# Performance work log

Measured on AMD Instinct MI355X. Metric: run time of the kernel, lower is better.

Reference implementation:

```python
import jax, jax.numpy as jnp
import numpy as np

B, S, E = 2, 2048, 2048
H, KV, D = 16, 4, 128
G = H // KV  # query heads per kv head
THETA = 10000.0


def setup_inputs() -> dict:
    key = jax.random.key(0)
    ks = jax.random.split(key, 5)
    scale = 0.02
    return {
        "x": jax.random.normal(ks[0], (B, S, E), dtype=jnp.float32),
        "Wq": jax.random.normal(ks[1], (E, H * D), dtype=jnp.float32) * scale,
        "Wk": jax.random.normal(ks[2], (E, KV * D), dtype=jnp.float32) * scale,
        "Wv": jax.random.normal(ks[3], (E, KV * D), dtype=jnp.float32) * scale,
        "Wo": jax.random.normal(ks[4], (E, E), dtype=jnp.float32) * scale,
    }


def _rope_tables(seq_len, head_dim, theta):
    inv_freq = 1.0 / theta ** (jnp.arange(0, head_dim, 2, dtype=jnp.float32) / head_dim)
    t = jnp.arange(seq_len, dtype=jnp.float32)
    freqs = jnp.outer(t, inv_freq)  # [S, D/2]
    cos = jnp.concatenate([jnp.cos(freqs), jnp.cos(freqs)], axis=-1)  # [S, D]
    sin = jnp.concatenate([jnp.sin(freqs), jnp.sin(freqs)], axis=-1)
    return cos, sin


def _apply_rope(x, cos, sin):
    # x: [B, h, S, D]; cos/sin: [S, D] broadcast over batch/heads
    d2 = x.shape[-1] // 2
    x1, x2 = x[..., :d2], x[..., d2:]
    rotated = jnp.concatenate([-x2, x1], axis=-1)
    return x * cos + rotated * sin


def reference(x, Wq, Wk, Wv, Wo):
    b, s, _ = x.shape
    q = (x @ Wq).reshape(b, s, H, D).transpose(0, 2, 1, 3)   # [B,H,S,D]
    k = (x @ Wk).reshape(b, s, KV, D).transpose(0, 2, 1, 3)  # [B,KV,S,D]
    v = (x @ Wv).reshape(b, s, KV, D).transpose(0, 2, 1, 3)

    cos, sin = _rope_tables(s, D, THETA)
    q = _apply_rope(q, cos, sin)
    k = _apply_rope(k, cos, sin)

    # GQA: q head h attends to kv head h // G (repeat_interleave order)
    qg = q.reshape(b, KV, G, s, D)
    scores = jnp.einsum("bkgsd,bktd->bkgst", qg, k) / jnp.sqrt(jnp.asarray(D, x.dtype))
    causal = jnp.tril(jnp.ones((s, s), dtype=bool))
    scores = jnp.where(causal, scores, jnp.asarray(-jnp.inf, scores.dtype))
    attn = jax.nn.softmax(scores, axis=-1)
    out = jnp.einsum("bkgst,bktd->bkgsd", attn, v)  # [B,KV,G,S,D]
    out = out.reshape(b, H, s, D).transpose(0, 2, 1, 3).reshape(b, s, H * D)
    return out @ Wo
```

## Files before the change

### kernel.cpp

```cpp
#include <hip/hip_runtime.h>
#include <stdint.h>

#define B_ 2
#define S_ 2048
#define E_ 2048
#define H_ 16
#define KV_ 4
#define D_ 128
#define G_ (H_ / KV_)
#define M_ (B_ * S_)

typedef unsigned short u16;
typedef unsigned int u32;
typedef __bf16 bf16x8 __attribute__((ext_vector_type(8)));
typedef float f32x4 __attribute__((ext_vector_type(4)));

__device__ __forceinline__ u16 f2bf(float f) {
  __bf16 h = (__bf16)f;
  return *(u16*)&h;
}
__device__ __forceinline__ float bf2f(u16 x) {
  return __uint_as_float(((u32)x) << 16);
}
__device__ __forceinline__ void store_c(u16* p, float v) { *p = f2bf(v); }
__device__ __forceinline__ void store_c(float* p, float v) { *p = v; }

__device__ __forceinline__ void gload_lds16(const u16* g, u16* lds) {
  __builtin_amdgcn_global_load_lds((const __attribute__((address_space(1))) u32*)g,
                                   (__attribute__((address_space(3))) u32*)lds,
                                   16, 0, 0);
}

__global__ __launch_bounds__(256) void convert_fp32_bf16(const float4* __restrict__ x,
                                                         uint2* __restrict__ o, int n4) {
  int i = blockIdx.x * 256 + threadIdx.x;
  if (i >= n4) return;
  float4 v = x[i];
  uint2 r;
  r.x = (u32)f2bf(v.x) | ((u32)f2bf(v.y) << 16);
  r.y = (u32)f2bf(v.z) | ((u32)f2bf(v.w) << 16);
  o[i] = r;
}

__global__ __launch_bounds__(256) void transpose_conv_w(const float* __restrict__ W,
                                                        u16* __restrict__ Wt,
                                                        int Kdim, int Ndim) {
  __shared__ float tile[32][33];
  int n0 = blockIdx.x * 32, k0 = blockIdx.y * 32;
  int tx = threadIdx.x, ty = threadIdx.y;
#pragma unroll
  for (int i = 0; i < 4; i++) {
    int r = ty + i * 8;
    tile[r][tx] = W[(size_t)(k0 + r) * Ndim + n0 + tx];
  }
  __syncthreads();
#pragma unroll
  for (int i = 0; i < 4; i++) {
    int r = ty + i * 8;
    Wt[(size_t)(n0 + r) * Kdim + k0 + tx] = f2bf(tile[tx][r]);
  }
}

__global__ __launch_bounds__(256) void transpose_v(const u16* __restrict__ V,
                                                   u16* __restrict__ Vt) {
  __shared__ u16 tile[32][33];
  int bkv = blockIdx.z;
  int b = bkv / KV_, kv = bkv % KV_;
  int s0 = blockIdx.x * 32, d0 = blockIdx.y * 32;
  int tx = threadIdx.x, ty = threadIdx.y;
#pragma unroll
  for (int i = 0; i < 4; i++) {
    int r = ty + i * 8;
    tile[r][tx] = V[((size_t)((b * S_ + s0 + r) * KV_ + kv)) * D_ + d0 + tx];
  }
  __syncthreads();
#pragma unroll
  for (int i = 0; i < 4; i++) {
    int r = ty + i * 8;
    Vt[((size_t)(b * KV_ + kv) * D_ + d0 + r) * S_ + s0 + tx] = tile[tx][r];
  }
}

__global__ __launch_bounds__(256) void rope_k_repack(const u16* __restrict__ Kin,
                                                     u16* __restrict__ Kp, int total) {
  int idx = blockIdx.x * 256 + threadIdx.x;
  if (idx >= total) return;
  int d = idx & 63;
  int rem = idx >> 6;
  int kv = rem % KV_;
  int row = rem / KV_;
  int b = row >> 11;
  int spos = row & (S_ - 1);
  size_t src = ((size_t)row * KV_ + kv) * D_ + d;
  float x0 = bf2f(Kin[src]);
  float x1 = bf2f(Kin[src + 64]);
  float ang = (float)spos * expf(-0.14391156831212787f * (float)d);
  float sn, cs;
  sincosf(ang, &sn, &cs);
  size_t dst = ((size_t)((b * KV_ + kv) * S_ + spos)) * D_ + d;
  Kp[dst]      = f2bf(x0 * cs - x1 * sn);
  Kp[dst + 64] = f2bf(x1 * cs + x0 * sn);
}

template <typename CT>
__device__ __forceinline__ void gemm_body(const u16* __restrict__ A, const u16* __restrict__ Bt,
                                          CT* __restrict__ C, int Kdim, int Ndim,
                                          int m0, int n0) {
  __shared__ __align__(16) u16 As[128 * 32];
  __shared__ __align__(16) u16 Bs[128 * 32];
  const int tid = threadIdx.x;
  const int lane = tid & 63;
  const int wave = tid >> 6;
  const int wm = wave >> 1, wn = wave & 1;
  const int quad = lane >> 4, lm = lane & 15;
  const int srow = tid >> 2;
  const int scol = (tid & 3) * 8;

  f32x4 zero = {0.f, 0.f, 0.f, 0.f};
  f32x4 acc[4][4];
#pragma unroll
  for (int i = 0; i < 4; i++)
#pragma unroll
    for (int j = 0; j < 4; j++) acc[i][j] = zero;

  const u16* gA = A + (size_t)(m0 + srow) * Kdim + scol;
  const u16* gB = Bt + (size_t)(n0 + srow) * Kdim + scol;
  const size_t rstep = (size_t)64 * Kdim;
  u16* ldsA0 = As + wave * 512;
  u16* ldsA1 = As + 2048 + wave * 512;
  u16* ldsB0 = Bs + wave * 512;
  u16* ldsB1 = Bs + 2048 + wave * 512;

  for (int k0 = 0; k0 < Kdim; k0 += 32) {
    gload_lds16(gA + k0, ldsA0);
    gload_lds16(gA + k0 + rstep, ldsA1);
    gload_lds16(gB + k0, ldsB0);
    gload_lds16(gB + k0 + rstep, ldsB1);
    __syncthreads();
    bf16x8 af[4], bfr[4];
#pragma unroll
    for (int mt = 0; mt < 4; mt++)
      af[mt] = *(const bf16x8*)(As + (wm * 64 + mt * 16 + lm) * 32 + quad * 8);
#pragma unroll
    for (int nt = 0; nt < 4; nt++)
      bfr[nt] = *(const bf16x8*)(Bs + (wn * 64 + nt * 16 + lm) * 32 + quad * 8);
#pragma unroll
    for (int mt = 0; mt < 4; mt++)
#pragma unroll
      for (int nt = 0; nt < 4; nt++)
        acc[mt][nt] = __builtin_amdgcn_mfma_f32_16x16x32_bf16(af[mt], bfr[nt], acc[mt][nt], 0, 0, 0);
    __syncthreads();
  }

#pragma unroll
  for (int mt = 0; mt < 4; mt++) {
    const int row = m0 + wm * 64 + mt * 16 + quad * 4;
#pragma unroll
    for (int nt = 0; nt < 4; nt++) {
      const int col = n0 + wn * 64 + nt * 16 + lm;
#pragma unroll
      for (int r = 0; r < 4; r++)
        store_c(C + (size_t)(row + r) * Ndim + col, acc[mt][nt][r]);
    }
  }
}

template <typename CT>
__global__ __launch_bounds__(256) void gemm_bt_kernel(const u16* __restrict__ A,
                                                      const u16* __restrict__ Bt,
                                                      CT* __restrict__ C, int Ndim, int Kdim) {
  gemm_body<CT>(A, Bt, C, Kdim, Ndim, blockIdx.y * 128, blockIdx.x * 128);
}

__global__ __launch_bounds__(256) void gemm_qkv_kernel(const u16* __restrict__ A,
                                                       const u16* __restrict__ WqT,
                                                       const u16* __restrict__ WkT,
                                                       const u16* __restrict__ WvT,
                                                       u16* __restrict__ Qb,
                                                       u16* __restrict__ Kb,
                                                       u16* __restrict__ Vb) {
  int bx = blockIdx.x;
  const u16* Bt;
  u16* C;
  int n0, Ndim;
  if (bx < 16)      { Bt = WqT; C = Qb; n0 = bx * 128;        Ndim = 2048; }
  else if (bx < 20) { Bt = WkT; C = Kb; n0 = (bx - 16) * 128; Ndim = 512; }
  else              { Bt = WvT; C = Vb; n0 = (bx - 20) * 128; Ndim = 512; }
  gemm_body<u16>(A, Bt, C, 2048, Ndim, blockIdx.y * 128, n0);
}

__global__ __launch_bounds__(256, 2) void attn_kernel(const u16* __restrict__ Q,
                                                      const u16* __restrict__ Kp,
                                                      const u16* __restrict__ Vt,
                                                      u16* __restrict__ O) {
  __shared__ __align__(16) u16 Ksh[2][64 * 128];
  __shared__ __align__(16) u16 Vsh[128 * 64];
  __shared__ __align__(16) u16 Psh[4][16 * 64];

  const int tid = threadIdx.x;
  const int lane = tid & 63;
  const int wave = tid >> 6;
  const int quad = lane >> 4, lm = lane & 15;
  const int b = blockIdx.z, h = blockIdx.y;
  const int kh = h / G_;

  const u16* Kbase = Kp + (size_t)(b * KV_ + kh) * S_ * D_;
  const u16* Vbase = Vt + (size_t)(b * KV_ + kh) * D_ * S_;
  u16* pw = &Psh[wave][0];

  int offK[4], offV[4], ldsOff[4];
#pragma unroll
  for (int i = 0; i < 4; i++) {
    int idx = (wave * 4 + i) * 64 + lane;
    int rK = idx >> 4;
    int cK = (idx & 15) ^ (rK & 7);
    offK[i] = rK * 128 + cK * 8;
    int rV = idx >> 3;
    int cV = (idx & 7) ^ (rV & 7);
    offV[i] = rV * S_ + cV * 8;
    ldsOff[i] = (wave * 4 + i) * 512;
  }

  bf16x8 onesb;
#pragma unroll
  for (int j = 0; j < 8; j++) onesb[j] = (__bf16)1.0f;

#pragma unroll
  for (int half = 0; half < 2; half++) {
    const int qi = half ? blockIdx.x : (31 - blockIdx.x);
    const int sq0 = qi * 64;
    const int nT = qi + 1;
    const int wrow = sq0 + wave * 16;

    const int spos = wrow + lm;
    const u16* qptr = Q + ((size_t)(b * S_ + wrow + lm) * H_ + h) * D_;
    bf16x8 qf[4];
#pragma unroll
    for (int ks = 0; ks < 2; ks++) {
      bf16x8 a = *(const bf16x8*)(qptr + ks * 32 + quad * 8);
      bf16x8 c = *(const bf16x8*)(qptr + (ks + 2) * 32 + quad * 8);
#pragma unroll
      for (int j = 0; j < 8; j++) {
        int d = ks * 32 + quad * 8 + j;
        float ang = (float)spos * __expf(-0.14391156831212787f * (float)d);
        float sn, cs;
        sincosf(ang, &sn, &cs);
        float x0 = (float)a[j], x1 = (float)c[j];
        const float scale = 0.08838834764831845f;
        qf[ks][j]     = (__bf16)((x0 * cs - x1 * sn) * scale);
        qf[ks + 2][j] = (__bf16)((x1 * cs + x0 * sn) * scale);
      }
    }

    f32x4 o[8];
    f32x4 lacc = {0.f, 0.f, 0.f, 0.f};
#pragma unroll
    for (int i = 0; i < 8; i++) o[i] = f32x4{0.f, 0.f, 0.f, 0.f};

    __syncthreads();
#pragma unroll
    for (int i = 0; i < 4; i++)
      gload_lds16(Kbase + offK[i], &Ksh[0][ldsOff[i]]);

    for (int t = 0; t < nT; t++) {
      const int sk0 = t << 6;
      const bool act = (sk0 <= wrow + 15);
      __syncthreads();

      if (t + 1 < nT) {
        const u16* kg = Kbase + (size_t)(t + 1) * 64 * 128;
        u16* kb_next = &Ksh[(t + 1) & 1][0];
#pragma unroll
        for (int i = 0; i < 4; i++)
          gload_lds16(kg + offK[i], kb_next + ldsOff[i]);
      }
#pragma unroll
      for (int i = 0; i < 4; i++)
        gload_lds16(Vbase + sk0 + offV[i], &Vsh[ldsOff[i]]);

      f32x4 sc[4];
      if (act) {
        const u16* kbuf = &Ksh[t & 1][0];
#pragma unroll
        for (int nt = 0; nt < 4; nt++) sc[nt] = f32x4{0.f, 0.f, 0.f, 0.f};
#pragma unroll
        for (int ks = 0; ks < 4; ks++) {
#pragma unroll
          for (int nt = 0; nt < 4; nt++) {
            int R = nt * 16 + lm;
            bf16x8 kb = *(const bf16x8*)(kbuf + R * 128 + (((ks * 4 + quad) ^ (R & 7)) * 8));
            sc[nt] = __builtin_amdgcn_mfma_f32_16x16x32_bf16(qf[ks], kb, sc[nt], 0, 0, 0);
          }
        }
#pragma unroll
        for (int nt = 0; nt < 4; nt++)
#pragma unroll
          for (int r = 0; r < 4; r++) {
            float p = __expf(sc[nt][r]);
            int kc = sk0 + nt * 16 + lm;
            int qr = wrow + quad * 4 + r;
            sc[nt][r] = (kc > qr) ? 0.f : p;
          }
#pragma unroll
        for (int nt = 0; nt < 4; nt++)
#pragma unroll
          for (int r = 0; r < 4; r++) {
            int p = quad * 4 + r;
            int c = nt * 2 + (lm >> 3);
            pw[p * 64 + ((c ^ (p & 7)) * 8) + (lm & 7)] = f2bf(sc[nt][r]);
          }
      }

      __syncthreads();

      if (act) {
#pragma unroll
        for (int ks = 0; ks < 2; ks++) {
          int pr = lm;
          bf16x8 pa = *(const bf16x8*)(pw + pr * 64 + (((ks * 4 + quad) ^ (pr & 7)) * 8));
          lacc = __builtin_amdgcn_mfma_f32_16x16x32_bf16(pa, onesb, lacc, 0, 0, 0);
#pragma unroll
          for (int d8 = 0; d8 < 8; d8++) {
            int R = d8 * 16 + lm;
            bf16x8 vb = *(const bf16x8*)(Vsh + R * 64 + (((ks * 4 + quad) ^ (R & 7)) * 8));
            o[d8] = __builtin_amdgcn_mfma_f32_16x16x32_bf16(pa, vb, o[d8], 0, 0, 0);
          }
        }
      }
    }

    float inv[4];
#pragma unroll
    for (int r = 0; r < 4; r++) inv[r] = 1.0f / lacc[r];
#pragma unroll
    for (int d8 = 0; d8 < 8; d8++)
#pragma unroll
      for (int r = 0; r < 4; r++) {
        int srow = wrow + quad * 4 + r;
        O[((size_t)(b * S_ + srow) * H_ + h) * D_ + d8 * 16 + lm] = f2bf(o[d8][r] * inv[r]);
      }
  }
}

extern "C" void kernel_launch(void* const* d_in, const int* in_sizes, int n_in,
                              void* d_out, int out_size, void* d_ws, size_t ws_size,
                              hipStream_t stream) {
  const float* x  = (const float*)d_in[0];
  const float* Wq = (const float*)d_in[1];
  const float* Wk = (const float*)d_in[2];
  const float* Wv = (const float*)d_in[3];
  const float* Wo = (const float*)d_in[4];
  float* out = (float*)d_out;
  char* ws = (char*)d_ws;
  u16* Xb  = (u16*)(ws);
  u16* WqT = (u16*)(ws + (16ull << 20));
  u16* WkT = (u16*)(ws + (24ull << 20));
  u16* WvT = (u16*)(ws + (26ull << 20));
  u16* WoT = (u16*)(ws + (28ull << 20));
  u16* Qb  = (u16*)(ws + (36ull << 20));
  u16* Kb  = (u16*)(ws + (52ull << 20));
  u16* Vb  = (u16*)(ws + (56ull << 20));
  u16* Vt  = (u16*)(ws + (60ull << 20));
  u16* Ob  = (u16*)(ws + (64ull << 20));
  u16* Kp  = (u16*)(ws + (80ull << 20));

  dim3 tb32(32, 8);

  convert_fp32_bf16<<<dim3(M_ * E_ / 4 / 256), 256, 0, stream>>>((const float4*)x, (uint2*)Xb, M_ * E_ / 4);
  transpose_conv_w<<<dim3(2048 / 32, 2048 / 32), tb32, 0, stream>>>(Wq, WqT, E_, H_ * D_);
  transpose_conv_w<<<dim3(512 / 32, 2048 / 32), tb32, 0, stream>>>(Wk, WkT, E_, KV_ * D_);
  transpose_conv_w<<<dim3(512 / 32, 2048 / 32), tb32, 0, stream>>>(Wv, WvT, E_, KV_ * D_);
  transpose_conv_w<<<dim3(2048 / 32, 2048 / 32), tb32, 0, stream>>>(Wo, WoT, E_, E_);

  gemm_qkv_kernel<<<dim3(24, M_ / 128), 256, 0, stream>>>(Xb, WqT, WkT, WvT, Qb, Kb, Vb);

  rope_k_repack<<<dim3(M_ * KV_ * 64 / 256), 256, 0, stream>>>(Kb, Kp, M_ * KV_ * 64);

  transpose_v<<<dim3(S_ / 32, D_ / 32, B_ * KV_), tb32, 0, stream>>>(Vb, Vt);

  attn_kernel<<<dim3(16, H_, B_), 256, 0, stream>>>(Qb, Kp, Vt, Ob);

  gemm_bt_kernel<float><<<dim3(2048 / 128, M_ / 128), 256, 0, stream>>>(Ob, WoT, out, 2048, 2048);
}
```

Baseline: 306.7 us.

## Replace 128x128 GEMMs with 256x256 double-buffered swizzled LDS pipeline

Rewrites the QKV and output-projection GEMMs as 256x256-tile, 512-thread kernels with a 64-wide K step. Operands are double-buffered in 128KB of dynamic LDS using XOR-swizzled layout, and global-to-LDS loads are interleaved with MFMA phases using barriers and s_setprio. The goal is more data reuse per tile, fewer LDS bank conflicts, and overlap of memory loads with compute. The trade-off is fewer blocks: the QKV GEMM gets 192 tiles and Wo gets 128 on a chip with 256 CUs, so occupancy and wave-quantization may suffer.

```diff
diff --git a/kernel.cpp b/kernel.cpp
--- a/kernel.cpp
+++ b/kernel.cpp
@@ -103,90 +103,175 @@
 }
 
 template <typename CT>
-__device__ __forceinline__ void gemm_body(const u16* __restrict__ A, const u16* __restrict__ Bt,
-                                          CT* __restrict__ C, int Kdim, int Ndim,
-                                          int m0, int n0) {
-  __shared__ __align__(16) u16 As[128 * 32];
-  __shared__ __align__(16) u16 Bs[128 * 32];
-  const int tid = threadIdx.x;
+__device__ __forceinline__ void gemm256_body(const u16* __restrict__ A,
+                                             const u16* __restrict__ Bt,
+                                             CT* __restrict__ C,
+                                             int Kdim, int Ndim, int m0, int n0) {
+  extern __shared__ __align__(16) u16 smem[];
+  const int tid  = threadIdx.x;
   const int lane = tid & 63;
   const int wave = tid >> 6;
-  const int wm = wave >> 1, wn = wave & 1;
+  const int wm   = wave >> 2;
+  const int wn   = wave & 3;
+  const int bh   = wn >> 1;
+  const int nb   = (wn & 1) * 64;
   const int quad = lane >> 4, lm = lane & 15;
-  const int srow = tid >> 2;
-  const int scol = (tid & 3) * 8;
-
+
+  int soff[2], sldb[2];
+#pragma unroll
+  for (int i = 0; i < 2; i++) {
+    int cc  = i * 512 + tid;
+    int row = cc >> 3;
+    int q   = (cc & 7) ^ (row & 7);
+    soff[i] = row * Kdim + q * 8;
+    sldb[i] = (i * 512 + wave * 64) * 8;
+  }
+  auto STAGE = [&](const u16* g, u16* l) {
+    gload_lds16(g + soff[0], l + sldb[0]);
+    gload_lds16(g + soff[1], l + sldb[1]);
+  };
+
+  int cs0 = ((0 + quad) ^ (lm & 7)) * 8;
+  int cs1 = ((4 + quad) ^ (lm & 7)) * 8;
+
+  const u16* Ag = A  + (size_t)m0 * Kdim;
+  const u16* Bg = Bt + (size_t)n0 * Kdim;
+  const size_t hstep = (size_t)128 * Kdim;
+
+  f32x4 acc[8][4];
   f32x4 zero = {0.f, 0.f, 0.f, 0.f};
-  f32x4 acc[4][4];
-#pragma unroll
-  for (int i = 0; i < 4; i++)
-#pragma unroll
-    for (int j = 0; j < 4; j++) acc[i][j] = zero;
-
-  const u16* gA = A + (size_t)(m0 + srow) * Kdim + scol;
-  const u16* gB = Bt + (size_t)(n0 + srow) * Kdim + scol;
-  const size_t rstep = (size_t)64 * Kdim;
-  u16* ldsA0 = As + wave * 512;
-  u16* ldsA1 = As + 2048 + wave * 512;
-  u16* ldsB0 = Bs + wave * 512;
-  u16* ldsB1 = Bs + 2048 + wave * 512;
-
-  for (int k0 = 0; k0 < Kdim; k0 += 32) {
-    gload_lds16(gA + k0, ldsA0);
-    gload_lds16(gA + k0 + rstep, ldsA1);
-    gload_lds16(gB + k0, ldsB0);
-    gload_lds16(gB + k0 + rstep, ldsB1);
-    __syncthreads();
-    bf16x8 af[4], bfr[4];
-#pragma unroll
-    for (int mt = 0; mt < 4; mt++)
-      af[mt] = *(const bf16x8*)(As + (wm * 64 + mt * 16 + lm) * 32 + quad * 8);
-#pragma unroll
-    for (int nt = 0; nt < 4; nt++)
-      bfr[nt] = *(const bf16x8*)(Bs + (wn * 64 + nt * 16 + lm) * 32 + quad * 8);
-#pragma unroll
-    for (int mt = 0; mt < 4; mt++)
-#pragma unroll
-      for (int nt = 0; nt < 4; nt++)
-        acc[mt][nt] = __builtin_amdgcn_mfma_f32_16x16x32_bf16(af[mt], bfr[nt], acc[mt][nt], 0, 0, 0);
-    __syncthreads();
-  }
-
-#pragma unroll
-  for (int mt = 0; mt < 4; mt++) {
-    const int row = m0 + wm * 64 + mt * 16 + quad * 4;
-#pragma unroll
-    for (int nt = 0; nt < 4; nt++) {
-      const int col = n0 + wn * 64 + nt * 16 + lm;
+#pragma unroll
+  for (int m = 0; m < 8; m++)
+#pragma unroll
+    for (int n = 0; n < 4; n++) acc[m][n] = zero;
+
+  const int NKT = Kdim >> 6;
+
+  STAGE(Bg,             smem + 32768 + 0 * 8192);
+  STAGE(Ag,             smem + 0 * 8192);
+  STAGE(Ag + hstep,     smem + 1 * 8192);
+  STAGE(Bg + hstep,     smem + 32768 + 1 * 8192);
+  STAGE(Bg + 64,        smem + 32768 + 2 * 8192);
+  STAGE(Ag + 64,        smem + 2 * 8192);
+  STAGE(Ag + hstep + 64, smem + 3 * 8192);
+  asm volatile("s_waitcnt vmcnt(6)" ::: "memory");
+  __builtin_amdgcn_s_barrier();
+
+  for (int kt = 0; kt < NKT; ++kt) {
+    const int cur = kt & 1;
+    const u16* regA = smem + (cur * 2 + wm) * 8192;
+    const u16* regB = smem + 32768 + (cur * 2 + bh) * 8192;
+    bf16x8 af[4][2], bf[4][2];
+
+#pragma unroll
+    for (int n = 0; n < 4; n++) {
+      bf[n][0] = *(const bf16x8*)(regB + (nb + n * 16 + lm) * 64 + cs0);
+      bf[n][1] = *(const bf16x8*)(regB + (nb + n * 16 + lm) * 64 + cs1);
+    }
+#pragma unroll
+    for (int m = 0; m < 4; m++) {
+      af[m][0] = *(const bf16x8*)(regA + (m * 16 + lm) * 64 + cs0);
+      af[m][1] = *(const bf16x8*)(regA + (m * 16 + lm) * 64 + cs1);
+    }
+    if (kt + 1 < NKT)
+      STAGE(Bg + hstep + (size_t)(kt + 1) * 64,
+            smem + 32768 + (((kt + 1) & 1) * 2 + 1) * 8192);
+    asm volatile("s_waitcnt lgkmcnt(0)" ::: "memory");
+    __builtin_amdgcn_s_barrier();
+    __builtin_amdgcn_s_setprio(1);
+#pragma unroll
+    for (int m = 0; m < 4; m++)
+#pragma unroll
+      for (int n = 0; n < 2; n++) {
+        acc[m][n] = __builtin_amdgcn_mfma_f32_16x16x32_bf16(af[m][0], bf[n][0], acc[m][n], 0, 0, 0);
+        acc[m][n] = __builtin_amdgcn_mfma_f32_16x16x32_bf16(af[m][1], bf[n][1], acc[m][n], 0, 0, 0);
+      }
+    __builtin_amdgcn_s_setprio(0);
+    __builtin_amdgcn_s_barrier();
+
+    if (kt + 2 < NKT)
+      STAGE(Bg + (size_t)(kt + 2) * 64, smem + 32768 + (cur * 2 + 0) * 8192);
+    __builtin_amdgcn_s_barrier();
+    __builtin_amdgcn_s_setprio(1);
+#pragma unroll
+    for (int m = 0; m < 4; m++)
+#pragma unroll
+      for (int n = 2; n < 4; n++) {
+        acc[m][n] = __builtin_amdgcn_mfma_f32_16x16x32_bf16(af[m][0], bf[n][0], acc[m][n], 0, 0, 0);
+        acc[m][n] = __builtin_amdgcn_mfma_f32_16x16x32_bf16(af[m][1], bf[n][1], acc[m][n], 0, 0, 0);
+      }
+    __builtin_amdgcn_s_setprio(0);
+    __builtin_amdgcn_s_barrier();
+
+#pragma unroll
+    for (int m = 0; m < 4; m++) {
+      af[m][0] = *(const bf16x8*)(regA + ((m + 4) * 16 + lm) * 64 + cs0);
+      af[m][1] = *(const bf16x8*)(regA + ((m + 4) * 16 + lm) * 64 + cs1);
+    }
+    asm volatile("s_waitcnt lgkmcnt(0)" ::: "memory");
+    __builtin_amdgcn_s_barrier();
+    __builtin_amdgcn_s_setprio(1);
+#pragma unroll
+    for (int m = 0; m < 4; m++)
+#pragma unroll
+      for (int n = 0; n < 2; n++) {
+        acc[m + 4][n] = __builtin_amdgcn_mfma_f32_16x16x32_bf16(af[m][0], bf[n][0], acc[m + 4][n], 0, 0, 0);
+        acc[m + 4][n] = __builtin_amdgcn_mfma_f32_16x16x32_bf16(af[m][1], bf[n][1], acc[m + 4][n], 0, 0, 0);
+      }
+    __builtin_amdgcn_s_setprio(0);
+    __builtin_amdgcn_s_barrier();
+
+    if (kt + 2 < NKT) {
+      STAGE(Ag + (size_t)(kt + 2) * 64,         smem + (cur * 2 + 0) * 8192);
+      STAGE(Ag + hstep + (size_t)(kt + 2) * 64, smem + (cur * 2 + 1) * 8192);
+    }
+    __builtin_amdgcn_s_setprio(1);
+#pragma unroll
+    for (int m = 0; m < 4; m++)
+#pragma unroll
+      for (int n = 2; n < 4; n++) {
+        acc[m + 4][n] = __builtin_amdgcn_mfma_f32_16x16x32_bf16(af[m][0], bf[n][0], acc[m + 4][n], 0, 0, 0);
+        acc[m + 4][n] = __builtin_amdgcn_mfma_f32_16x16x32_bf16(af[m][1], bf[n][1], acc[m + 4][n], 0, 0, 0);
+      }
+    __builtin_amdgcn_s_setprio(0);
+    asm volatile("s_waitcnt vmcnt(6)" ::: "memory");
+    __builtin_amdgcn_s_barrier();
+  }
+
+#pragma unroll
+  for (int m = 0; m < 8; m++) {
+    const int row = m0 + wm * 128 + m * 16 + quad * 4;
+#pragma unroll
+    for (int n = 0; n < 4; n++) {
+      const int col = n0 + wn * 64 + n * 16 + lm;
 #pragma unroll
       for (int r = 0; r < 4; r++)
-        store_c(C + (size_t)(row + r) * Ndim + col, acc[mt][nt][r]);
-    }
-  }
-}
-
-template <typename CT>
-__global__ __launch_bounds__(256) void gemm_bt_kernel(const u16* __restrict__ A,
-                                                      const u16* __restrict__ Bt,
-                                                      CT* __restrict__ C, int Ndim, int Kdim) {
-  gemm_body<CT>(A, Bt, C, Kdim, Ndim, blockIdx.y * 128, blockIdx.x * 128);
-}
-
-__global__ __launch_bounds__(256) void gemm_qkv_kernel(const u16* __restrict__ A,
-                                                       const u16* __restrict__ WqT,
-                                                       const u16* __restrict__ WkT,
-                                                       const u16* __restrict__ WvT,
-                                                       u16* __restrict__ Qb,
-                                                       u16* __restrict__ Kb,
-                                                       u16* __restrict__ Vb) {
+        store_c(C + (size_t)(row + r) * Ndim + col, acc[m][n][r]);
+    }
+  }
+}
+
+__global__ __launch_bounds__(512, 2) void gemm256_qkv(const u16* __restrict__ A,
+                                                      const u16* __restrict__ WqT,
+                                                      const u16* __restrict__ WkT,
+                                                      const u16* __restrict__ WvT,
+                                                      u16* __restrict__ Qb,
+                                                      u16* __restrict__ Kb,
+                                                      u16* __restrict__ Vb) {
   int bx = blockIdx.x;
   const u16* Bt;
   u16* C;
   int n0, Ndim;
-  if (bx < 16)      { Bt = WqT; C = Qb; n0 = bx * 128;        Ndim = 2048; }
-  else if (bx < 20) { Bt = WkT; C = Kb; n0 = (bx - 16) * 128; Ndim = 512; }
-  else              { Bt = WvT; C = Vb; n0 = (bx - 20) * 128; Ndim = 512; }
-  gemm_body<u16>(A, Bt, C, 2048, Ndim, blockIdx.y * 128, n0);
+  if (bx < 8)       { Bt = WqT; C = Qb; n0 = bx * 256;        Ndim = 2048; }
+  else if (bx < 10) { Bt = WkT; C = Kb; n0 = (bx - 8) * 256;  Ndim = 512; }
+  else              { Bt = WvT; C = Vb; n0 = (bx - 10) * 256; Ndim = 512; }
+  gemm256_body<u16>(A, Bt, C, 2048, Ndim, blockIdx.y * 256, n0);
+}
+
+__global__ __launch_bounds__(512, 2) void gemm256_wo(const u16* __restrict__ A,
+                                                     const u16* __restrict__ Bt,
+                                                     float* __restrict__ C) {
+  gemm256_body<float>(A, Bt, C, 2048, 2048, blockIdx.y * 256, blockIdx.x * 256);
 }
 
 __global__ __launch_bounds__(256, 2) void attn_kernel(const u16* __restrict__ Q,
@@ -364,6 +449,15 @@
   u16* Ob  = (u16*)(ws + (64ull << 20));
   u16* Kp  = (u16*)(ws + (80ull << 20));
 
+  static bool attr_set = false;
+  if (!attr_set) {
+    hipFuncSetAttribute((const void*)gemm256_qkv,
+                        hipFuncAttributeMaxDynamicSharedMemorySize, 131072);
+    hipFuncSetAttribute((const void*)gemm256_wo,
+                        hipFuncAttributeMaxDynamicSharedMemorySize, 131072);
+    attr_set = true;
+  }
+
   dim3 tb32(32, 8);
 
   convert_fp32_bf16<<<dim3(M_ * E_ / 4 / 256), 256, 0, stream>>>((const float4*)x, (uint2*)Xb, M_ * E_ / 4);
@@ -372,7 +466,7 @@
   transpose_conv_w<<<dim3(512 / 32, 2048 / 32), tb32, 0, stream>>>(Wv, WvT, E_, KV_ * D_);
   transpose_conv_w<<<dim3(2048 / 32, 2048 / 32), tb32, 0, stream>>>(Wo, WoT, E_, E_);
 
-  gemm_qkv_kernel<<<dim3(24, M_ / 128), 256, 0, stream>>>(Xb, WqT, WkT, WvT, Qb, Kb, Vb);
+  gemm256_qkv<<<dim3(12, M_ / 256), 512, 131072, stream>>>(Xb, WqT, WkT, WvT, Qb, Kb, Vb);
 
   rope_k_repack<<<dim3(M_ * KV_ * 64 / 256), 256, 0, stream>>>(Kb, Kp, M_ * KV_ * 64);
 
@@ -380,5 +474,5 @@
 
   attn_kernel<<<dim3(16, H_, B_), 256, 0, stream>>>(Qb, Kp, Vt, Ob);
 
-  gemm_bt_kernel<float><<<dim3(2048 / 128, M_ / 128), 256, 0, stream>>>(Ob, WoT, out, 2048, 2048);
-}
+  gemm256_wo<<<dim3(2048 / 256, M_ / 256), 512, 131072, stream>>>(Ob, WoT, out);
+}
```

After: 316.5 us. +3.2%, slower.
